# Kernel optimization log

Measured on AMD Instinct MI355X. Metric: run time of the kernel, lower is better.

## Reference

```python
import jax, jax.numpy as jnp
import numpy as np

NUM_LAYERS = 5
EMB_DIM = 300
NUM_ATOM_TYPE = 121
NUM_CHIRALITY = 11
NUM_BOND_TYPE = 7
NUM_BOND_DIR = 3
BN_EPS = 1e-5


def setup_inputs() -> dict:
    key = jax.random.key(0)
    ks = jax.random.split(key, 16)
    N, E, D, L = 100000, 200000, EMB_DIM, NUM_LAYERS

    def glorot(k, shape):
        fan_in, fan_out = shape[-2], shape[-1]
        s = jnp.sqrt(6.0 / (fan_in + fan_out))
        return jax.random.uniform(k, shape, jnp.float32, -s, s)

    x = jax.random.randint(ks[0], (N, 2), 0, 11)  # atom type / chirality (both < 11, in range)
    edge_index = jax.random.randint(ks[1], (2, E), 0, N)
    edge_attr = jax.random.randint(ks[2], (E, 2), 0, 3)

    return {
        "x": x,
        "edge_index": edge_index,
        "edge_attr": edge_attr,
        "x_emb1": glorot(ks[3], (NUM_ATOM_TYPE, D)),
        "x_emb2": glorot(ks[4], (NUM_CHIRALITY, D)),
        "edge_emb1": glorot(ks[5], (L, NUM_BOND_TYPE, D)),
        "edge_emb2": glorot(ks[6], (L, NUM_BOND_DIR, D)),
        "w1": glorot(ks[7], (L, D, 2 * D)),
        "b1": jnp.zeros((L, 2 * D), jnp.float32),
        "w2": glorot(ks[8], (L, 2 * D, D)),
        "b2": jnp.zeros((L, D), jnp.float32),
        "bn_gamma": jnp.ones((L, D), jnp.float32),
        "bn_beta": jnp.zeros((L, D), jnp.float32),
    }


def reference(x, edge_index, edge_attr, x_emb1, x_emb2, edge_emb1, edge_emb2,
              w1, b1, w2, b2, bn_gamma, bn_beta):
    N = x.shape[0]
    # GINConv.forward adds self loops with edge_attr row [4, 0]
    loop = jnp.arange(N)
    src = jnp.concatenate([edge_index[0], loop])  # [E+N]
    dst = jnp.concatenate([edge_index[1], loop])  # [E+N]
    ea0 = jnp.concatenate([edge_attr[:, 0], jnp.full((N,), 4, edge_attr.dtype)])
    ea1 = jnp.concatenate([edge_attr[:, 1], jnp.zeros((N,), edge_attr.dtype)])

    # node input embedding
    h = x_emb1[x[:, 0]] + x_emb2[x[:, 1]]  # [N, D]

    for l in range(NUM_LAYERS):
        # edge embeddings (incl. self loops)
        eemb = edge_emb1[l][ea0] + edge_emb2[l][ea1]  # [E+N, D]
        # message: x_j + edge_attr, aggr='add' at destination nodes
        msg = h[src] + eemb
        agg = jax.ops.segment_sum(msg, dst, num_segments=N)  # [N, D]
        # GIN update MLP: Linear(D, 2D) -> ReLU -> Linear(2D, D)
        h2 = jax.nn.relu(agg @ w1[l] + b1[l]) @ w2[l] + b2[l]
        # BatchNorm1d (training mode: batch statistics, biased variance)
        mean = h2.mean(axis=0)
        var = h2.var(axis=0)
        h2 = (h2 - mean) * jax.lax.rsqrt(var + BN_EPS) * bn_gamma[l] + bn_beta[l]
        # ReLU on all but last layer (dropout is identity, drop_ratio=0)
        if l < NUM_LAYERS - 1:
            h2 = jax.nn.relu(h2)
        h = h2
    # JK == 'last'
    return h
```

## Files before the change

kernel.cpp:

```cpp
#include <hip/hip_runtime.h>
#include <hip/hip_bf16.h>
#include <stdint.h>

typedef __bf16 bf16_t;
typedef bf16_t bf16x8 __attribute__((ext_vector_type(8)));
typedef bf16_t bf16x4 __attribute__((ext_vector_type(4)));
typedef float  f32x4  __attribute__((ext_vector_type(4)));

__global__ void embed_kernel(const int* __restrict__ x, const float* __restrict__ e1,
                             const float* __restrict__ e2, bf16_t* __restrict__ h, int N) {
  const int w = (blockIdx.x * blockDim.x + threadIdx.x) >> 6;
  const int lane = threadIdx.x & 63;
  if (w >= N || lane >= 40) return;
  const int t0 = x[2 * w], t1 = x[2 * w + 1];
  const int co = lane * 8;
  f32x4 a0 = *(const f32x4*)&e1[t0 * 300 + co];
  f32x4 a1 = *(const f32x4*)&e1[t0 * 300 + co + 4];
  f32x4 b0 = *(const f32x4*)&e2[t1 * 300 + co];
  f32x4 b1 = *(const f32x4*)&e2[t1 * 300 + co + 4];
  bf16x8 o;
  #pragma unroll
  for (int j = 0; j < 8; j++) {
    float v = (j < 4) ? (a0[j] + b0[j]) : (a1[j - 4] + b1[j - 4]);
    o[j] = (co + j < 300) ? (bf16_t)v : (bf16_t)0.f;
  }
  *(bf16x8*)&h[(size_t)w * 320 + co] = o;
}

__global__ void count_deg_kernel(const int* __restrict__ ei, int* __restrict__ deg, int E) {
  int e = blockIdx.x * 256 + threadIdx.x;
  if (e < E) atomicAdd(&deg[ei[E + e]], 1);
}

__global__ void scan_partial_kernel(const int* __restrict__ deg, int* __restrict__ part, int N) {
  __shared__ int s[256];
  const int tid = threadIdx.x;
  const int idx = blockIdx.x * 256 + tid;
  s[tid] = (idx < N) ? deg[idx] : 0;
  __syncthreads();
  for (int off = 128; off > 0; off >>= 1) {
    if (tid < off) s[tid] += s[tid + off];
    __syncthreads();
  }
  if (tid == 0) part[blockIdx.x] = s[0];
}

__global__ void scan_block_kernel(int* __restrict__ part, int n) {
  __shared__ int s[1024];
  const int tid = threadIdx.x;
  const int v = (tid < n) ? part[tid] : 0;
  s[tid] = v;
  __syncthreads();
  for (int off = 1; off < 1024; off <<= 1) {
    int x = (tid >= off) ? s[tid - off] : 0;
    __syncthreads();
    s[tid] += x;
    __syncthreads();
  }
  if (tid < n) part[tid] = s[tid] - v;
}

__global__ void scan_final_kernel(const int* __restrict__ deg, const int* __restrict__ part,
                                  int* __restrict__ rowptr, int* __restrict__ cursor, int N, int E) {
  __shared__ int s[256];
  const int tid = threadIdx.x;
  const int idx = blockIdx.x * 256 + tid;
  const int v = (idx < N) ? deg[idx] : 0;
  s[tid] = v;
  __syncthreads();
  for (int off = 1; off < 256; off <<= 1) {
    int x = (tid >= off) ? s[tid - off] : 0;
    __syncthreads();
    s[tid] += x;
    __syncthreads();
  }
  if (idx < N) {
    int ex = s[tid] - v + part[blockIdx.x];
    rowptr[idx] = ex;
    cursor[idx] = ex;
  }
  if (idx == 0) rowptr[N] = E;
}

__global__ void fill_csr_kernel(const int* __restrict__ ei, const int* __restrict__ ea,
                                int* __restrict__ cursor, int* __restrict__ epack, int E) {
  int e = blockIdx.x * 256 + threadIdx.x;
  if (e >= E) return;
  int slot = atomicAdd(&cursor[ei[E + e]], 1);
  int a = ea[2 * e] * 3 + ea[2 * e + 1];
  epack[slot] = (ei[e] & 0xFFFFF) | (a << 20);
}

__global__ void convert_w1_kernel(const float* __restrict__ w1, bf16_t* __restrict__ o) {
  int id = blockIdx.x * 256 + threadIdx.x;
  if (id >= 5 * 40 * 10 * 512) return;
  int j = id & 7;
  int lane = (id >> 3) & 63;
  int rest = id >> 9;
  int ks = rest % 10;
  int nt = (rest / 10) % 40;
  int l = rest / 400;
  int ml = lane & 15, quad = lane >> 4;
  int n = nt * 16 + ml;
  int k = ks * 32 + quad * 8 + j;
  float v = (k < 300 && n < 600) ? w1[((size_t)l * 300 + k) * 600 + n] : 0.f;
  o[id] = (bf16_t)v;
}

__global__ void convert_w2_kernel(const float* __restrict__ w2, bf16_t* __restrict__ o) {
  int id = blockIdx.x * 256 + threadIdx.x;
  if (id >= 5 * 24 * 20 * 512) return;
  int j = id & 7;
  int lane = (id >> 3) & 63;
  int rest = id >> 9;
  int ks = rest % 20;
  int nt = (rest / 20) % 24;
  int l = rest / 480;
  int ml = lane & 15, quad = lane >> 4;
  int n = nt * 16 + ml;
  int k = ks * 32 + quad * 8 + j;
  float v = (k < 600 && n < 300) ? w2[((size_t)l * 600 + k) * 300 + n] : 0.f;
  o[id] = (bf16_t)v;
}

__global__ void pad_bias_kernel(const float* __restrict__ b1, const float* __restrict__ b2,
                                float* __restrict__ b1p, float* __restrict__ b2p) {
  int t = blockIdx.x * 256 + threadIdx.x;
  if (t < 5 * 640) {
    int l = t / 640, n = t % 640;
    b1p[t] = (n < 600) ? b1[l * 600 + n] : 0.f;
  }
  if (t < 5 * 384) {
    int l = t / 384, n = t % 384;
    b2p[t] = (n < 300) ? b2[l * 300 + n] : 0.f;
  }
}

__global__ void build_t12_kernel(const float* __restrict__ ee1, const float* __restrict__ ee2,
                                 bf16_t* __restrict__ T12) {
  int id = blockIdx.x * 256 + threadIdx.x;
  if (id >= 5 * 21 * 320) return;
  int col = id % 320;
  int r = id / 320;
  int l = r / 21;
  int a = r % 21;
  int a0 = a / 3, a1 = a % 3;
  float v = 0.f;
  if (col < 300) v = ee1[((size_t)l * 7 + a0) * 300 + col] + ee2[((size_t)l * 3 + a1) * 300 + col];
  T12[id] = (bf16_t)v;
}

template <bool FUSE_BN>
__global__ void aggregate_kernel(const bf16_t* __restrict__ hsrc, const int* __restrict__ rowptr,
                                 const int* __restrict__ epack, const bf16_t* __restrict__ T12L,
                                 const float* __restrict__ scale, const float* __restrict__ shift,
                                 bf16_t* __restrict__ agg, int N, int LDH) {
  const int g = blockIdx.x * 256 + threadIdx.x;
  const int w = g / 40;
  if (w >= N) return;
  const int co = (g - w * 40) * 8;

  float sc[8], sh[8];
  if (FUSE_BN) {
    f32x4 s0 = *(const f32x4*)&scale[co];
    f32x4 s1 = *(const f32x4*)&scale[co + 4];
    f32x4 t0 = *(const f32x4*)&shift[co];
    f32x4 t1 = *(const f32x4*)&shift[co + 4];
    #pragma unroll
    for (int j = 0; j < 4; j++) { sc[j] = s0[j]; sc[j + 4] = s1[j]; sh[j] = t0[j]; sh[j + 4] = t1[j]; }
  }

  const int beg = rowptr[w], end = rowptr[w + 1];
  float acc[8];
  {
    bf16x8 hv = *(const bf16x8*)&hsrc[(size_t)w * LDH + co];
    bf16x8 tv = *(const bf16x8*)&T12L[12 * 320 + co];
    #pragma unroll
    for (int j = 0; j < 8; j++) {
      float v = (float)hv[j];
      if (FUSE_BN) v = fmaxf(v * sc[j] + sh[j], 0.f);
      acc[j] = v + (float)tv[j];
    }
  }
  for (int e = beg; e < end; e++) {
    const int p = epack[e];
    const int s = p & 0xFFFFF;
    const int a = (p >> 20) & 0x1F;
    bf16x8 hv = *(const bf16x8*)&hsrc[(size_t)s * LDH + co];
    bf16x8 tv = *(const bf16x8*)&T12L[a * 320 + co];
    #pragma unroll
    for (int j = 0; j < 8; j++) {
      float v = (float)hv[j];
      if (FUSE_BN) v = fmaxf(v * sc[j] + sh[j], 0.f);
      acc[j] += v + (float)tv[j];
    }
  }
  bf16x8 o;
  #pragma unroll
  for (int j = 0; j < 8; j++) o[j] = (bf16_t)acc[j];
  *(bf16x8*)&agg[(size_t)w * 320 + co] = o;
}

__global__ __launch_bounds__(512, 4) void fused_mlp_kernel(
    const bf16_t* __restrict__ agg,
    const bf16_t* __restrict__ W1f,
    const bf16_t* __restrict__ W2f,
    const float* __restrict__ b1p,
    const float* __restrict__ b2p,
    bf16_t* __restrict__ H2,
    float* __restrict__ sums, float* __restrict__ sumsq, int Nvalid) {
  __shared__ __align__(16) bf16_t As[10 * 64 * 32];
  __shared__ __align__(16) bf16_t C1pA[64 * 128];
  __shared__ __align__(16) bf16_t C1pB[64 * 128];

  const int tid = threadIdx.x;
  const int lane = tid & 63;
  const int w = tid >> 6;
  const int ml = lane & 15, quad = lane >> 4;
  const int kx = (ml >> 1) & 3;
  const int k7 = ml & 7;
  const int rg = w >> 2, cg = w & 3;
  const size_t bm = (size_t)blockIdx.x * 64;

  #pragma unroll
  for (int it = 0; it < 5; it++) {
    const int s = it * 512 + tid;
    const int ks = s >> 8;
    const int u = s & 255;
    const int row = u >> 2;
    const int cgl = (u & 3) ^ ((u >> 3) & 3);
    bf16x8 v = *(const bf16x8*)&agg[(bm + row) * 320 + ks * 32 + cgl * 8];
    *(bf16x8*)&As[(size_t)s * 8] = v;
  }
  asm volatile("s_waitcnt lgkmcnt(0)" ::: "memory");
  __builtin_amdgcn_s_barrier();
  __builtin_amdgcn_sched_barrier(0);

  f32x4 acc2[4][3];
  #pragma unroll
  for (int mf = 0; mf < 4; mf++)
    #pragma unroll
    for (int nf = 0; nf < 3; nf++) acc2[mf][nf] = (f32x4){0.f, 0.f, 0.f, 0.f};

  auto phase1 = [&](int c, bf16_t* dst) {
    f32x4 a1[2][2];
    #pragma unroll
    for (int mi = 0; mi < 2; mi++)
      #pragma unroll
      for (int ni = 0; ni < 2; ni++) a1[mi][ni] = (f32x4){0.f, 0.f, 0.f, 0.f};
    const int nt0 = c * 8 + cg * 2;
    #pragma unroll
    for (int ks = 0; ks < 10; ks++) {
      bf16x8 w1f0 = *(const bf16x8*)&W1f[(((size_t)nt0 * 10 + ks) * 64 + lane) * 8];
      bf16x8 w1f1 = *(const bf16x8*)&W1f[(((size_t)(nt0 + 1) * 10 + ks) * 64 + lane) * 8];
      #pragma unroll
      for (int mi = 0; mi < 2; mi++) {
        bf16x8 aF = *(const bf16x8*)&As[((ks * 64 + rg * 32 + mi * 16 + ml) * 4 + (quad ^ kx)) * 8];
        a1[mi][0] = __builtin_amdgcn_mfma_f32_16x16x32_bf16(w1f0, aF, a1[mi][0], 0, 0, 0);
        a1[mi][1] = __builtin_amdgcn_mfma_f32_16x16x32_bf16(w1f1, aF, a1[mi][1], 0, 0, 0);
      }
    }
    #pragma unroll
    for (int mi = 0; mi < 2; mi++) {
      const int row = rg * 32 + mi * 16 + ml;
      #pragma unroll
      for (int ni = 0; ni < 2; ni++) {
        const int colb = cg * 32 + ni * 16 + quad * 4;
        f32x4 bv = *(const f32x4*)&b1p[c * 128 + colb];
        bf16x4 o;
        #pragma unroll
        for (int i = 0; i < 4; i++) o[i] = (bf16_t)fmaxf(a1[mi][ni][i] + bv[i], 0.f);
        const int ls = colb >> 3;
        const int off = colb & 7;
        *(bf16x4*)&dst[row * 128 + ((ls ^ k7) * 8) + off] = o;
      }
    }
  };

  auto phase2 = [&](int c, const bf16_t* src) {
    #pragma unroll
    for (int ks2 = 0; ks2 < 4; ks2++) {
      bf16x8 c1f[4];
      #pragma unroll
      for (int mf = 0; mf < 4; mf++) {
        const int row = mf * 16 + ml;
        const int ls = ks2 * 4 + quad;
        c1f[mf] = *(const bf16x8*)&src[row * 128 + ((ls ^ k7) * 8)];
      }
      #pragma unroll
      for (int nf = 0; nf < 3; nf++) {
        bf16x8 w2f = *(const bf16x8*)&W2f[(((size_t)(w * 3 + nf) * 20 + c * 4 + ks2) * 64 + lane) * 8];
        #pragma unroll
        for (int mf = 0; mf < 4; mf++)
          acc2[mf][nf] = __builtin_amdgcn_mfma_f32_16x16x32_bf16(c1f[mf], w2f, acc2[mf][nf], 0, 0, 0);
      }
    }
  };

  phase1(0, C1pA);
  asm volatile("s_waitcnt lgkmcnt(0)" ::: "memory");
  __builtin_amdgcn_s_barrier();
  __builtin_amdgcn_sched_barrier(0);

  #pragma unroll
  for (int c = 0; c < 5; c++) {
    bf16_t* cur = (c & 1) ? C1pB : C1pA;
    bf16_t* oth = (c & 1) ? C1pA : C1pB;
    if (c < 4) phase1(c + 1, oth);
    phase2(c, cur);
    asm volatile("s_waitcnt lgkmcnt(0)" ::: "memory");
    __builtin_amdgcn_s_barrier();
    __builtin_amdgcn_sched_barrier(0);
  }

  #pragma unroll
  for (int nf = 0; nf < 3; nf++) {
    const int colg = (w * 3 + nf) * 16 + ml;
    const float bv = b2p[colg];
    float s = 0.f, sq = 0.f;
    #pragma unroll
    for (int mf = 0; mf < 4; mf++) {
      #pragma unroll
      for (int i = 0; i < 4; i++) {
        const size_t rowg = bm + mf * 16 + quad * 4 + i;
        float v = acc2[mf][nf][i] + bv;
        H2[rowg * 384 + colg] = (bf16_t)v;
        const bool ok = rowg < (size_t)Nvalid;
        s += ok ? v : 0.f;
        sq += ok ? v * v : 0.f;
      }
    }
    s += __shfl_down(s, 16);
    sq += __shfl_down(sq, 16);
    s += __shfl_down(s, 32);
    sq += __shfl_down(sq, 32);
    if (quad == 0) {
      atomicAdd(&sums[colg], s);
      atomicAdd(&sumsq[colg], sq);
    }
  }
}

__global__ void bn_params_kernel(const float* __restrict__ sums, const float* __restrict__ sumsq,
                                 const float* __restrict__ gamma, const float* __restrict__ beta,
                                 float* __restrict__ scale, float* __restrict__ shift, int N) {
  const int col = threadIdx.x;
  if (col >= 384) return;
  if (col >= 300) {
    scale[col] = 0.f;
    shift[col] = 0.f;
    return;
  }
  const float inv = 1.f / (float)N;
  const float mean = sums[col] * inv;
  float var = sumsq[col] * inv - mean * mean;
  if (var < 0.f) var = 0.f;
  const float sc = gamma[col] * rsqrtf(var + 1e-5f);
  scale[col] = sc;
  shift[col] = beta[col] - mean * sc;
}

__global__ void bn_apply_kernel(const bf16_t* __restrict__ H2, const float* __restrict__ scale,
                                const float* __restrict__ shift, float* __restrict__ out, int N) {
  const int w = (blockIdx.x * blockDim.x + threadIdx.x) >> 6;
  const int lane = threadIdx.x & 63;
  if (w >= N || lane >= 40) return;
  const int co = lane * 8;
  bf16x8 v8 = *(const bf16x8*)&H2[(size_t)w * 384 + co];
  f32x4 s0 = *(const f32x4*)&scale[co];
  f32x4 s1 = *(const f32x4*)&scale[co + 4];
  f32x4 t0 = *(const f32x4*)&shift[co];
  f32x4 t1 = *(const f32x4*)&shift[co + 4];
  #pragma unroll
  for (int j = 0; j < 8; j++) {
    float sc = (j < 4) ? s0[j] : s1[j - 4];
    float sh = (j < 4) ? t0[j] : t1[j - 4];
    float v = (float)v8[j] * sc + sh;
    if (co + j < 300) out[(size_t)w * 300 + co + j] = v;
  }
}

extern "C" void kernel_launch(void* const* d_in, const int* in_sizes, int n_in,
                              void* d_out, int out_size, void* d_ws, size_t ws_size,
                              hipStream_t stream) {
  const int* x = (const int*)d_in[0];
  const int* ei = (const int*)d_in[1];
  const int* ea = (const int*)d_in[2];
  const float* xe1 = (const float*)d_in[3];
  const float* xe2 = (const float*)d_in[4];
  const float* ee1 = (const float*)d_in[5];
  const float* ee2 = (const float*)d_in[6];
  const float* w1 = (const float*)d_in[7];
  const float* b1 = (const float*)d_in[8];
  const float* w2 = (const float*)d_in[9];
  const float* b2 = (const float*)d_in[10];
  const float* gam = (const float*)d_in[11];
  const float* bet = (const float*)d_in[12];

  const int N = in_sizes[0] / 2;
  const int E = in_sizes[1] / 2;
  const int Mt = (N + 127) / 128;
  const size_t Mp = (size_t)Mt * 128;
  const int Mt2 = (int)(Mp / 64);

  char* p = (char*)d_ws;
  auto take = [&](size_t b) -> char* {
    char* r = p;
    p += (b + 255) & ~(size_t)255;
    return r;
  };
  bf16_t* h    = (bf16_t*)take(Mp * 320 * 2);
  bf16_t* agg  = (bf16_t*)take(Mp * 320 * 2);
  bf16_t* H2   = (bf16_t*)take(Mp * 384 * 2);
  bf16_t* W1f  = (bf16_t*)take((size_t)5 * 40 * 10 * 512 * 2);
  bf16_t* W2f  = (bf16_t*)take((size_t)5 * 24 * 20 * 512 * 2);
  bf16_t* T12  = (bf16_t*)take((size_t)5 * 21 * 320 * 2);
  float* b1p   = (float*)take((size_t)5 * 640 * 4);
  float* b2p   = (float*)take((size_t)5 * 384 * 4);
  int* deg     = (int*)take((size_t)N * 4);
  int* rowptr  = (int*)take((size_t)(N + 1) * 4);
  int* cursor  = (int*)take((size_t)N * 4);
  int* part    = (int*)take(1024 * 4);
  int* epack   = (int*)take((size_t)E * 4);
  float* sums  = (float*)take(384 * 4);
  float* sumsq = (float*)take(384 * 4);
  float* scale = (float*)take(384 * 4);
  float* shift = (float*)take(384 * 4);

  hipMemsetAsync(agg, 0, Mp * 320 * 2, stream);
  hipMemsetAsync(deg, 0, (size_t)N * 4, stream);

  const int nwb = (N + 3) / 4;
  embed_kernel<<<nwb, 256, 0, stream>>>(x, xe1, xe2, h, N);

  count_deg_kernel<<<(E + 255) / 256, 256, 0, stream>>>(ei, deg, E);
  const int nsb = (N + 255) / 256;
  scan_partial_kernel<<<nsb, 256, 0, stream>>>(deg, part, N);
  scan_block_kernel<<<1, 1024, 0, stream>>>(part, nsb);
  scan_final_kernel<<<nsb, 256, 0, stream>>>(deg, part, rowptr, cursor, N, E);
  fill_csr_kernel<<<(E + 255) / 256, 256, 0, stream>>>(ei, ea, cursor, epack, E);

  convert_w1_kernel<<<(5 * 40 * 10 * 512 + 255) / 256, 256, 0, stream>>>(w1, W1f);
  convert_w2_kernel<<<(5 * 24 * 20 * 512 + 255) / 256, 256, 0, stream>>>(w2, W2f);
  pad_bias_kernel<<<(5 * 640 + 255) / 256, 256, 0, stream>>>(b1, b2, b1p, b2p);
  build_t12_kernel<<<(5 * 21 * 320 + 255) / 256, 256, 0, stream>>>(ee1, ee2, T12);

  const int nab = (N * 40 + 255) / 256;

  for (int l = 0; l < 5; l++) {
    if (l == 0) {
      aggregate_kernel<false><<<nab, 256, 0, stream>>>(h, rowptr, epack,
                                                       T12 + (size_t)l * 21 * 320,
                                                       scale, shift, agg, N, 320);
    } else {
      aggregate_kernel<true><<<nab, 256, 0, stream>>>(H2, rowptr, epack,
                                                      T12 + (size_t)l * 21 * 320,
                                                      scale, shift, agg, N, 384);
    }
    hipMemsetAsync(sums, 0, 384 * 4, stream);
    hipMemsetAsync(sumsq, 0, 384 * 4, stream);
    fused_mlp_kernel<<<Mt2, 512, 0, stream>>>(
        agg, W1f + (size_t)l * 40 * 10 * 512, W2f + (size_t)l * 24 * 20 * 512,
        b1p + (size_t)l * 640, b2p + (size_t)l * 384, H2, sums, sumsq, N);
    bn_params_kernel<<<1, 384, 0, stream>>>(sums, sumsq, gam + (size_t)l * 300,
                                            bet + (size_t)l * 300, scale, shift, N);
  }
  bn_apply_kernel<<<nwb, 256, 0, stream>>>(H2, scale, shift, (float*)d_out, N);
}
```

Measured before the change: 1.300 ms.

## Write aggregate output in MFMA fragment layout and drop LDS staging in MLP

The aggregate kernel now stores its output directly in the per-16-row MFMA fragment order that the first GEMM consumes. The fused MLP kernel then reads A fragments straight from global memory instead of staging a 64x320 tile in LDS behind a barrier. This removes the LDS copy, its barrier and 40KB of shared memory, which may allow higher occupancy. In exchange, A fragments are reloaded from global/L2 for each of the 5 column chunks, and the aggregate stores become more scattered.

```diff
diff --git a/kernel.cpp b/kernel.cpp
--- a/kernel.cpp
+++ b/kernel.cpp
@@ -154,7 +154,7 @@
 __global__ void aggregate_kernel(const bf16_t* __restrict__ hsrc, const int* __restrict__ rowptr,
                                  const int* __restrict__ epack, const bf16_t* __restrict__ T12L,
                                  const float* __restrict__ scale, const float* __restrict__ shift,
-                                 bf16_t* __restrict__ agg, int N, int LDH) {
+                                 bf16_t* __restrict__ Af, int N, int LDH) {
   const int g = blockIdx.x * 256 + threadIdx.x;
   const int w = g / 40;
   if (w >= N) return;
@@ -198,18 +198,19 @@
   bf16x8 o;
   #pragma unroll
   for (int j = 0; j < 8; j++) o[j] = (bf16_t)acc[j];
-  *(bf16x8*)&agg[(size_t)w * 320 + co] = o;
+  const int rb = w >> 4, mlw = w & 15;
+  const int ks = co >> 5, qd = (co >> 3) & 3;
+  *(bf16x8*)&Af[(((size_t)rb * 10 + ks) * 64 + qd * 16 + mlw) * 8] = o;
 }
 
 __global__ __launch_bounds__(512, 4) void fused_mlp_kernel(
-    const bf16_t* __restrict__ agg,
+    const bf16_t* __restrict__ Af,
     const bf16_t* __restrict__ W1f,
     const bf16_t* __restrict__ W2f,
     const float* __restrict__ b1p,
     const float* __restrict__ b2p,
     bf16_t* __restrict__ H2,
     float* __restrict__ sums, float* __restrict__ sumsq, int Nvalid) {
-  __shared__ __align__(16) bf16_t As[10 * 64 * 32];
   __shared__ __align__(16) bf16_t C1pA[64 * 128];
   __shared__ __align__(16) bf16_t C1pB[64 * 128];
 
@@ -217,24 +218,10 @@
   const int lane = tid & 63;
   const int w = tid >> 6;
   const int ml = lane & 15, quad = lane >> 4;
-  const int kx = (ml >> 1) & 3;
   const int k7 = ml & 7;
   const int rg = w >> 2, cg = w & 3;
+  const int rb0 = blockIdx.x * 4;
   const size_t bm = (size_t)blockIdx.x * 64;
-
-  #pragma unroll
-  for (int it = 0; it < 5; it++) {
-    const int s = it * 512 + tid;
-    const int ks = s >> 8;
-    const int u = s & 255;
-    const int row = u >> 2;
-    const int cgl = (u & 3) ^ ((u >> 3) & 3);
-    bf16x8 v = *(const bf16x8*)&agg[(bm + row) * 320 + ks * 32 + cgl * 8];
-    *(bf16x8*)&As[(size_t)s * 8] = v;
-  }
-  asm volatile("s_waitcnt lgkmcnt(0)" ::: "memory");
-  __builtin_amdgcn_s_barrier();
-  __builtin_amdgcn_sched_barrier(0);
 
   f32x4 acc2[4][3];
   #pragma unroll
@@ -255,7 +242,7 @@
       bf16x8 w1f1 = *(const bf16x8*)&W1f[(((size_t)(nt0 + 1) * 10 + ks) * 64 + lane) * 8];
       #pragma unroll
       for (int mi = 0; mi < 2; mi++) {
-        bf16x8 aF = *(const bf16x8*)&As[((ks * 64 + rg * 32 + mi * 16 + ml) * 4 + (quad ^ kx)) * 8];
+        bf16x8 aF = *(const bf16x8*)&Af[(((size_t)(rb0 + rg * 2 + mi) * 10 + ks) * 64 + lane) * 8];
         a1[mi][0] = __builtin_amdgcn_mfma_f32_16x16x32_bf16(w1f0, aF, a1[mi][0], 0, 0, 0);
         a1[mi][1] = __builtin_amdgcn_mfma_f32_16x16x32_bf16(w1f1, aF, a1[mi][1], 0, 0, 0);
       }
@@ -410,7 +397,7 @@
     return r;
   };
   bf16_t* h    = (bf16_t*)take(Mp * 320 * 2);
-  bf16_t* agg  = (bf16_t*)take(Mp * 320 * 2);
+  bf16_t* Af   = (bf16_t*)take(Mp * 320 * 2);
   bf16_t* H2   = (bf16_t*)take(Mp * 384 * 2);
   bf16_t* W1f  = (bf16_t*)take((size_t)5 * 40 * 10 * 512 * 2);
   bf16_t* W2f  = (bf16_t*)take((size_t)5 * 24 * 20 * 512 * 2);
@@ -427,7 +414,7 @@
   float* scale = (float*)take(384 * 4);
   float* shift = (float*)take(384 * 4);
 
-  hipMemsetAsync(agg, 0, Mp * 320 * 2, stream);
+  hipMemsetAsync(Af, 0, Mp * 320 * 2, stream);
   hipMemsetAsync(deg, 0, (size_t)N * 4, stream);
 
   const int nwb = (N + 3) / 4;
@@ -451,16 +438,16 @@
     if (l == 0) {
       aggregate_kernel<false><<<nab, 256, 0, stream>>>(h, rowptr, epack,
                                                        T12 + (size_t)l * 21 * 320,
-                                                       scale, shift, agg, N, 320);
+                                                       scale, shift, Af, N, 320);
     } else {
       aggregate_kernel<true><<<nab, 256, 0, stream>>>(H2, rowptr, epack,
                                                       T12 + (size_t)l * 21 * 320,
-                                                      scale, shift, agg, N, 384);
+                                                      scale, shift, Af, N, 384);
     }
     hipMemsetAsync(sums, 0, 384 * 4, stream);
     hipMemsetAsync(sumsq, 0, 384 * 4, stream);
     fused_mlp_kernel<<<Mt2, 512, 0, stream>>>(
-        agg, W1f + (size_t)l * 40 * 10 * 512, W2f + (size_t)l * 24 * 20 * 512,
+        Af, W1f + (size_t)l * 40 * 10 * 512, W2f + (size_t)l * 24 * 20 * 512,
         b1p + (size_t)l * 640, b2p + (size_t)l * 384, H2, sums, sumsq, N);
     bn_params_kernel<<<1, 384, 0, stream>>>(sums, sumsq, gam + (size_t)l * 300,
                                             bet + (size_t)l * 300, scale, shift, N);
```

Measured after the change: 1.486 ms. 14.3% more time.

## Shrink fused MLP row tile from 64 to 32 rows per block

Applied to the files above, without the earlier changes.

Halves the row tile of the fused two-layer MLP kernel: each block now handles 32 node rows, and each of the 8 waves computes one 16-column slice in phase 1 instead of a 2x2 fragment grid. Shared memory and accumulator registers per block are halved, launch bounds are raised to allow 8 blocks per CU, and the grid doubles. The aim is higher occupancy and more blocks for latency hiding. The cost is that each W1/W2 fragment load from global/L2 now feeds half as many MFMAs, so weight traffic per row doubles.

```diff
diff --git a/kernel.cpp b/kernel.cpp
--- a/kernel.cpp
+++ b/kernel.cpp
@@ -201,7 +201,7 @@
   *(bf16x8*)&agg[(size_t)w * 320 + co] = o;
 }
 
-__global__ __launch_bounds__(512, 4) void fused_mlp_kernel(
+__global__ __launch_bounds__(512, 8) void fused_mlp_kernel(
     const bf16_t* __restrict__ agg,
     const bf16_t* __restrict__ W1f,
     const bf16_t* __restrict__ W2f,
@@ -209,9 +209,9 @@
     const float* __restrict__ b2p,
     bf16_t* __restrict__ H2,
     float* __restrict__ sums, float* __restrict__ sumsq, int Nvalid) {
-  __shared__ __align__(16) bf16_t As[10 * 64 * 32];
-  __shared__ __align__(16) bf16_t C1pA[64 * 128];
-  __shared__ __align__(16) bf16_t C1pB[64 * 128];
+  __shared__ __align__(16) bf16_t As[10 * 32 * 32];
+  __shared__ __align__(16) bf16_t C1pA[32 * 128];
+  __shared__ __align__(16) bf16_t C1pB[32 * 128];
 
   const int tid = threadIdx.x;
   const int lane = tid & 63;
@@ -219,70 +219,73 @@
   const int ml = lane & 15, quad = lane >> 4;
   const int kx = (ml >> 1) & 3;
   const int k7 = ml & 7;
-  const int rg = w >> 2, cg = w & 3;
-  const size_t bm = (size_t)blockIdx.x * 64;
-
-  #pragma unroll
-  for (int it = 0; it < 5; it++) {
-    const int s = it * 512 + tid;
-    const int ks = s >> 8;
-    const int u = s & 255;
-    const int row = u >> 2;
-    const int cgl = (u & 3) ^ ((u >> 3) & 3);
-    bf16x8 v = *(const bf16x8*)&agg[(bm + row) * 320 + ks * 32 + cgl * 8];
-    *(bf16x8*)&As[(size_t)s * 8] = v;
+  const size_t bm = (size_t)blockIdx.x * 32;
+
+  {
+    int s = tid;
+    #pragma unroll
+    for (int it = 0; it < 2; it++) {
+      const int ks = s >> 7;
+      const int u = s & 127;
+      const int row = u >> 2;
+      const int cg = (u & 3) ^ ((u >> 3) & 3);
+      *(bf16x8*)&As[(size_t)s * 8] =
+          *(const bf16x8*)&agg[(bm + row) * 320 + ks * 32 + cg * 8];
+      s += 512;
+    }
+    if (tid < 256) {
+      const int ks = s >> 7;
+      const int u = s & 127;
+      const int row = u >> 2;
+      const int cg = (u & 3) ^ ((u >> 3) & 3);
+      *(bf16x8*)&As[(size_t)s * 8] =
+          *(const bf16x8*)&agg[(bm + row) * 320 + ks * 32 + cg * 8];
+    }
   }
   asm volatile("s_waitcnt lgkmcnt(0)" ::: "memory");
   __builtin_amdgcn_s_barrier();
   __builtin_amdgcn_sched_barrier(0);
 
-  f32x4 acc2[4][3];
-  #pragma unroll
-  for (int mf = 0; mf < 4; mf++)
+  f32x4 acc2[2][3];
+  #pragma unroll
+  for (int mf = 0; mf < 2; mf++)
     #pragma unroll
     for (int nf = 0; nf < 3; nf++) acc2[mf][nf] = (f32x4){0.f, 0.f, 0.f, 0.f};
 
   auto phase1 = [&](int c, bf16_t* dst) {
-    f32x4 a1[2][2];
-    #pragma unroll
-    for (int mi = 0; mi < 2; mi++)
-      #pragma unroll
-      for (int ni = 0; ni < 2; ni++) a1[mi][ni] = (f32x4){0.f, 0.f, 0.f, 0.f};
-    const int nt0 = c * 8 + cg * 2;
+    f32x4 a1[2];
+    a1[0] = (f32x4){0.f, 0.f, 0.f, 0.f};
+    a1[1] = (f32x4){0.f, 0.f, 0.f, 0.f};
+    const int nt = c * 8 + w;
     #pragma unroll
     for (int ks = 0; ks < 10; ks++) {
-      bf16x8 w1f0 = *(const bf16x8*)&W1f[(((size_t)nt0 * 10 + ks) * 64 + lane) * 8];
-      bf16x8 w1f1 = *(const bf16x8*)&W1f[(((size_t)(nt0 + 1) * 10 + ks) * 64 + lane) * 8];
+      bf16x8 w1f = *(const bf16x8*)&W1f[(((size_t)nt * 10 + ks) * 64 + lane) * 8];
       #pragma unroll
       for (int mi = 0; mi < 2; mi++) {
-        bf16x8 aF = *(const bf16x8*)&As[((ks * 64 + rg * 32 + mi * 16 + ml) * 4 + (quad ^ kx)) * 8];
-        a1[mi][0] = __builtin_amdgcn_mfma_f32_16x16x32_bf16(w1f0, aF, a1[mi][0], 0, 0, 0);
-        a1[mi][1] = __builtin_amdgcn_mfma_f32_16x16x32_bf16(w1f1, aF, a1[mi][1], 0, 0, 0);
+        bf16x8 aF = *(const bf16x8*)&As[((ks * 32 + mi * 16 + ml) * 4 + (quad ^ kx)) * 8];
+        a1[mi] = __builtin_amdgcn_mfma_f32_16x16x32_bf16(w1f, aF, a1[mi], 0, 0, 0);
       }
     }
+    const int colb = w * 16 + quad * 4;
+    f32x4 bv = *(const f32x4*)&b1p[c * 128 + colb];
+    const int ls = colb >> 3;
+    const int off = colb & 7;
     #pragma unroll
     for (int mi = 0; mi < 2; mi++) {
-      const int row = rg * 32 + mi * 16 + ml;
+      const int row = mi * 16 + ml;
+      bf16x4 o;
       #pragma unroll
-      for (int ni = 0; ni < 2; ni++) {
-        const int colb = cg * 32 + ni * 16 + quad * 4;
-        f32x4 bv = *(const f32x4*)&b1p[c * 128 + colb];
-        bf16x4 o;
-        #pragma unroll
-        for (int i = 0; i < 4; i++) o[i] = (bf16_t)fmaxf(a1[mi][ni][i] + bv[i], 0.f);
-        const int ls = colb >> 3;
-        const int off = colb & 7;
-        *(bf16x4*)&dst[row * 128 + ((ls ^ k7) * 8) + off] = o;
-      }
+      for (int i = 0; i < 4; i++) o[i] = (bf16_t)fmaxf(a1[mi][i] + bv[i], 0.f);
+      *(bf16x4*)&dst[row * 128 + ((ls ^ k7) * 8) + off] = o;
     }
   };
 
   auto phase2 = [&](int c, const bf16_t* src) {
     #pragma unroll
     for (int ks2 = 0; ks2 < 4; ks2++) {
-      bf16x8 c1f[4];
+      bf16x8 c1f[2];
       #pragma unroll
-      for (int mf = 0; mf < 4; mf++) {
+      for (int mf = 0; mf < 2; mf++) {
         const int row = mf * 16 + ml;
         const int ls = ks2 * 4 + quad;
         c1f[mf] = *(const bf16x8*)&src[row * 128 + ((ls ^ k7) * 8)];
@@ -291,7 +294,7 @@
       for (int nf = 0; nf < 3; nf++) {
         bf16x8 w2f = *(const bf16x8*)&W2f[(((size_t)(w * 3 + nf) * 20 + c * 4 + ks2) * 64 + lane) * 8];
         #pragma unroll
-        for (int mf = 0; mf < 4; mf++)
+        for (int mf = 0; mf < 2; mf++)
           acc2[mf][nf] = __builtin_amdgcn_mfma_f32_16x16x32_bf16(c1f[mf], w2f, acc2[mf][nf], 0, 0, 0);
       }
     }
@@ -319,7 +322,7 @@
     const float bv = b2p[colg];
     float s = 0.f, sq = 0.f;
     #pragma unroll
-    for (int mf = 0; mf < 4; mf++) {
+    for (int mf = 0; mf < 2; mf++) {
       #pragma unroll
       for (int i = 0; i < 4; i++) {
         const size_t rowg = bm + mf * 16 + quad * 4 + i;
@@ -401,7 +404,7 @@
   const int E = in_sizes[1] / 2;
   const int Mt = (N + 127) / 128;
   const size_t Mp = (size_t)Mt * 128;
-  const int Mt2 = (int)(Mp / 64);
+  const int Mt2 = (int)(Mp / 32);
 
   char* p = (char*)d_ws;
   auto take = [&](size_t b) -> char* {
```

Result: slower. 1.502 ms (+15.5%).

## Stage MLP output through LDS for vectorized stores and cache first A fragments

Applied to the files above, without the earlier changes.

The MLP kernel's epilogue now writes H2 into a padded shared-memory scratch area instead of issuing scattered 2-byte global stores. After a barrier, each thread writes 16-byte vectors, so global writes become coalesced. Shared memory is merged into one buffer so the scratch can reuse the A and C1 space. The first four K-slices of the A fragments are also kept in registers across all phase1 calls, cutting repeated LDS reads at the cost of more registers, which may lower occupancy.

```diff
diff --git a/kernel.cpp b/kernel.cpp
--- a/kernel.cpp
+++ b/kernel.cpp
@@ -209,9 +209,10 @@
     const float* __restrict__ b2p,
     bf16_t* __restrict__ H2,
     float* __restrict__ sums, float* __restrict__ sumsq, int Nvalid) {
-  __shared__ __align__(16) bf16_t As[10 * 64 * 32];
-  __shared__ __align__(16) bf16_t C1pA[64 * 128];
-  __shared__ __align__(16) bf16_t C1pB[64 * 128];
+  __shared__ __align__(16) bf16_t SH[36864];
+  bf16_t* As   = SH;
+  bf16_t* C1pA = SH + 20480;
+  bf16_t* C1pB = SH + 28672;
 
   const int tid = threadIdx.x;
   const int lane = tid & 63;
@@ -236,6 +237,13 @@
   __builtin_amdgcn_s_barrier();
   __builtin_amdgcn_sched_barrier(0);
 
+  bf16x8 aH[2][4];
+  #pragma unroll
+  for (int mi = 0; mi < 2; mi++)
+    #pragma unroll
+    for (int ks = 0; ks < 4; ks++)
+      aH[mi][ks] = *(const bf16x8*)&As[((ks * 64 + rg * 32 + mi * 16 + ml) * 4 + (quad ^ kx)) * 8];
+
   f32x4 acc2[4][3];
   #pragma unroll
   for (int mf = 0; mf < 4; mf++)
@@ -255,7 +263,9 @@
       bf16x8 w1f1 = *(const bf16x8*)&W1f[(((size_t)(nt0 + 1) * 10 + ks) * 64 + lane) * 8];
       #pragma unroll
       for (int mi = 0; mi < 2; mi++) {
-        bf16x8 aF = *(const bf16x8*)&As[((ks * 64 + rg * 32 + mi * 16 + ml) * 4 + (quad ^ kx)) * 8];
+        bf16x8 aF = (ks < 4)
+            ? aH[mi][ks & 3]
+            : *(const bf16x8*)&As[((ks * 64 + rg * 32 + mi * 16 + ml) * 4 + (quad ^ kx)) * 8];
         a1[mi][0] = __builtin_amdgcn_mfma_f32_16x16x32_bf16(w1f0, aF, a1[mi][0], 0, 0, 0);
         a1[mi][1] = __builtin_amdgcn_mfma_f32_16x16x32_bf16(w1f1, aF, a1[mi][1], 0, 0, 0);
       }
@@ -313,6 +323,7 @@
     __builtin_amdgcn_sched_barrier(0);
   }
 
+  bf16_t* scr = SH;
   #pragma unroll
   for (int nf = 0; nf < 3; nf++) {
     const int colg = (w * 3 + nf) * 16 + ml;
@@ -322,10 +333,10 @@
     for (int mf = 0; mf < 4; mf++) {
       #pragma unroll
       for (int i = 0; i < 4; i++) {
-        const size_t rowg = bm + mf * 16 + quad * 4 + i;
+        const int rowl = mf * 16 + quad * 4 + i;
         float v = acc2[mf][nf][i] + bv;
-        H2[rowg * 384 + colg] = (bf16_t)v;
-        const bool ok = rowg < (size_t)Nvalid;
+        scr[rowl * 392 + colg] = (bf16_t)v;
+        const bool ok = bm + rowl < (size_t)Nvalid;
         s += ok ? v : 0.f;
         sq += ok ? v * v : 0.f;
       }
@@ -337,6 +348,18 @@
     if (quad == 0) {
       atomicAdd(&sums[colg], s);
       atomicAdd(&sumsq[colg], sq);
+    }
+  }
+  asm volatile("s_waitcnt lgkmcnt(0)" ::: "memory");
+  __builtin_amdgcn_s_barrier();
+  __builtin_amdgcn_sched_barrier(0);
+  {
+    const int orow = tid >> 3;
+    const int ocol = (tid & 7) * 48;
+    #pragma unroll
+    for (int j = 0; j < 6; j++) {
+      bf16x8 v8 = *(const bf16x8*)&scr[orow * 392 + ocol + j * 8];
+      *(bf16x8*)&H2[(bm + orow) * 384 + ocol + j * 8] = v8;
     }
   }
 }
```

Measured after the change: 1.534 ms. 1.18x slower.
